# Optimization experiments

Hardware: AMD Instinct MI355X
Metric: run time of the kernel (lower is better)

Reference implementation:

```python
import jax, jax.numpy as jnp
import numpy as np

D_MODEL = 1024
N_HEAD = 16
D_HEAD = D_MODEL // N_HEAD
N_EXPERTS = 8
TOP_K = 2
D_FF = 4096
EPS = 1e-6


def setup_inputs() -> dict:
    key = jax.random.key(0)
    ks = jax.random.split(key, 16)
    s = 0.02  # init scale
    d, dff, E = D_MODEL, D_FF, N_EXPERTS
    return {
        "dec": jax.random.normal(ks[0], (4, 1024, d), jnp.float32),
        "text_encoder": jax.random.normal(ks[1], (4, 512, d), jnp.float32),
        # self-attention projections
        "Wq1": jax.random.normal(ks[2], (d, d), jnp.float32) * s,
        "Wk1": jax.random.normal(ks[3], (d, d), jnp.float32) * s,
        "Wv1": jax.random.normal(ks[4], (d, d), jnp.float32) * s,
        "Wo1": jax.random.normal(ks[5], (d, d), jnp.float32) * s,
        # cross-attention projections
        "Wq2": jax.random.normal(ks[6], (d, d), jnp.float32) * s,
        "Wk2": jax.random.normal(ks[7], (d, d), jnp.float32) * s,
        "Wv2": jax.random.normal(ks[8], (d, d), jnp.float32) * s,
        "Wo2": jax.random.normal(ks[9], (d, d), jnp.float32) * s,
        # shared RMSNorm gain (module uses one norm instance three times)
        "g": jnp.ones((d,), jnp.float32),
        # MoE router + per-expert FFN weights
        "Wg": jax.random.normal(ks[10], (d, E), jnp.float32) * s,
        "W1": jax.random.normal(ks[11], (E, d, dff), jnp.float32) * s,
        "W2": jax.random.normal(ks[12], (E, dff, d), jnp.float32) * s,
    }


def rmsnorm(x, g):
    return x * jax.lax.rsqrt(jnp.mean(x * x, axis=-1, keepdims=True) + EPS) * g


def mha(q_in, k_in, v_in, Wq, Wk, Wv, Wo):
    B, Sq, _ = q_in.shape
    Sk = k_in.shape[1]
    q = (q_in @ Wq).reshape(B, Sq, N_HEAD, D_HEAD)
    k = (k_in @ Wk).reshape(B, Sk, N_HEAD, D_HEAD)
    v = (v_in @ Wv).reshape(B, Sk, N_HEAD, D_HEAD)
    scores = jnp.einsum("bqhd,bkhd->bhqk", q, k) / jnp.sqrt(jnp.asarray(D_HEAD, q.dtype))
    attn = jax.nn.softmax(scores, axis=-1)
    out = jnp.einsum("bhqk,bkhd->bqhd", attn, v).reshape(B, Sq, D_MODEL)
    return out @ Wo


def moe(x, Wg, W1, W2):
    # top-k softmax router, renormalized weights; dense per-expert FFN with combine
    probs = jax.nn.softmax(x @ Wg, axis=-1)              # [B,S,E]
    weights, indices = jax.lax.top_k(probs, TOP_K)        # [B,S,k]
    weights = weights / jnp.sum(weights, axis=-1, keepdims=True)
    # combine[t,e] = sum_k weights[t,k] * (indices[t,k]==e)
    combine = jnp.sum(
        jax.nn.one_hot(indices, N_EXPERTS, dtype=x.dtype) * weights[..., None], axis=-2
    )  # [B,S,E]
    out = jnp.zeros_like(x)
    for e in range(N_EXPERTS):  # fixed small expert loop
        h = jax.nn.relu(x @ W1[e]) @ W2[e]
        out = out + combine[..., e:e + 1] * h
    return weights, indices, out


def reference(dec, text_encoder, Wq1, Wk1, Wv1, Wo1, Wq2, Wk2, Wv2, Wo2, g, Wg, W1, W2):
    # self-attention + residual + RMSNorm (dropout p=0 -> identity)
    x = rmsnorm(mha(dec, dec, dec, Wq1, Wk1, Wv1, Wo1) + dec, g)
    # cross-attention + residual + RMSNorm
    x = rmsnorm(mha(x, text_encoder, text_encoder, Wq2, Wk2, Wv2, Wo2) + x, g)
    # MoE FFN + residual + RMSNorm
    weights, indices, y = moe(x, Wg, W1, W2)
    x = rmsnorm(y + x, g)
    return weights, indices, x
```

## Files before the change

### kernel.cpp

```cpp
#include <hip/hip_runtime.h>
#include <stdint.h>

#define D_    1024
#define BB    4
#define SDEC  1024
#define STXT  512
#define TDEC  4096
#define TTXT  2048
#define NH    16
#define DHD   64
#define NE    8
#define DFF   4096
#define NSLOT 8192
#define ND1   8192
#define ND2   4096
#define MOEGRID 512

using u16 = unsigned short;
typedef __attribute__((ext_vector_type(8))) short bf16x8;
typedef __attribute__((ext_vector_type(4))) float f32x4;

__device__ __forceinline__ float bf2f(u16 h) {
    union { unsigned int u; float f; } x; x.u = ((unsigned int)h) << 16; return x.f;
}
__device__ __forceinline__ u16 f2bf(float f) {
    union { float f; unsigned int u; } x; x.f = f;
    unsigned int lsb = (x.u >> 16) & 1u;
    return (u16)((x.u + 0x7fffu + lsb) >> 16);
}

__device__ __forceinline__ void gld16(const u16* g, u16* l) {
    __builtin_amdgcn_global_load_lds((const __attribute__((address_space(1))) void*)g,
                                     (__attribute__((address_space(3))) void*)l,
                                     16, 0, 0);
}

constexpr int BM = 128, BK = 32;

template<int SPLIT, int EPI, int BROWS>
__global__ __launch_bounds__(256) void gemm_bt(
    const u16* __restrict__ AH, const u16* __restrict__ AL,
    const u16* __restrict__ BH, const u16* __restrict__ BL,
    float* __restrict__ Cf, u16* __restrict__ CH, u16* __restrict__ CL,
    int M, int N, int K, int lda, int ldb, int ldc, int nb2,
    long strA1, long strA2, long strB1, long strB2, long strC1, long strC2)
{
    constexpr int WM = (BROWS == 64) ? 2 : 4;
    constexpr int ASZ = BM * BK, BSZ = BROWS * BK;
    __shared__ u16 smem[(SPLIT ? 2 : 1) * (ASZ + BSZ)];
    u16* sAH = smem;
    u16* sBH = smem + ASZ;
    u16* sAL = SPLIT ? smem + ASZ + BSZ : nullptr;
    u16* sBL = SPLIT ? smem + 2 * ASZ + BSZ : nullptr;

    const int z = blockIdx.z;
    const int z1 = z / nb2, z2 = z % nb2;
    const long zA = (long)z1 * strA1 + (long)z2 * strA2;
    const long zB = (long)z1 * strB1 + (long)z2 * strB2;
    const long zC = (long)z1 * strC1 + (long)z2 * strC2;

    const int tileM = blockIdx.y * BM, tileN = blockIdx.x * BROWS;
    const int t = threadIdx.x;
    const int sr = t >> 2;
    const int sc = (t & 3) << 3;
    const u16* pA = AH + zA + (long)(tileM + sr) * lda + sc;
    const u16* pB = BH + zB + (long)(tileN + sr) * ldb + sc;
    const u16* pAl = nullptr; const u16* pBl = nullptr;
    if constexpr (SPLIT) {
        pAl = AL + zA + (long)(tileM + sr) * lda + sc;
        pBl = BL + zB + (long)(tileN + sr) * ldb + sc;
    }
    const long hA = 64L * lda, hB = 64L * ldb;

    const int lane = t & 63;
    const int wv = t >> 6;
    const int wr = (BROWS == 64) ? (wv << 5) : ((wv >> 1) << 6);
    const int wc = (BROWS == 64) ? 0 : ((wv & 1) << 6);
    const int fr = lane & 15, kg = lane >> 4;

    f32x4 acc[WM][4];
    const f32x4 vzero = {0.f, 0.f, 0.f, 0.f};
#pragma unroll
    for (int m = 0; m < WM; ++m)
#pragma unroll
        for (int n = 0; n < 4; ++n) acc[m][n] = vzero;

    for (int k0 = 0; k0 < K; k0 += BK) {
        gld16(pA + k0,      sAH + t * 8);
        gld16(pA + k0 + hA, sAH + 2048 + t * 8);
        gld16(pB + k0,      sBH + t * 8);
        if constexpr (BROWS == 128) gld16(pB + k0 + hB, sBH + 2048 + t * 8);
        if constexpr (SPLIT) {
            gld16(pAl + k0,      sAL + t * 8);
            gld16(pAl + k0 + hA, sAL + 2048 + t * 8);
            gld16(pBl + k0,      sBL + t * 8);
            if constexpr (BROWS == 128) gld16(pBl + k0 + hB, sBL + 2048 + t * 8);
        }
        __syncthreads();

        bf16x8 fa[WM], fb[4], fal[WM], fbl[4];
#pragma unroll
        for (int m = 0; m < WM; ++m) {
            fa[m] = *(const bf16x8*)&sAH[(wr + m * 16 + fr) * BK + (kg << 3)];
            if constexpr (SPLIT) fal[m] = *(const bf16x8*)&sAL[(wr + m * 16 + fr) * BK + (kg << 3)];
        }
#pragma unroll
        for (int n = 0; n < 4; ++n) {
            fb[n] = *(const bf16x8*)&sBH[(wc + n * 16 + fr) * BK + (kg << 3)];
            if constexpr (SPLIT) fbl[n] = *(const bf16x8*)&sBL[(wc + n * 16 + fr) * BK + (kg << 3)];
        }
#pragma unroll
        for (int m = 0; m < WM; ++m)
#pragma unroll
            for (int n = 0; n < 4; ++n) {
                acc[m][n] = __builtin_amdgcn_mfma_f32_16x16x32_bf16(fa[m], fb[n], acc[m][n], 0, 0, 0);
                if constexpr (SPLIT) {
                    acc[m][n] = __builtin_amdgcn_mfma_f32_16x16x32_bf16(fa[m],  fbl[n], acc[m][n], 0, 0, 0);
                    acc[m][n] = __builtin_amdgcn_mfma_f32_16x16x32_bf16(fal[m], fb[n],  acc[m][n], 0, 0, 0);
                }
            }
        __syncthreads();
    }

#pragma unroll
    for (int m = 0; m < WM; ++m) {
        const int r0 = tileM + wr + m * 16 + (kg << 2);
#pragma unroll
        for (int n = 0; n < 4; ++n) {
            const int col = tileN + wc + n * 16 + fr;
            if (col >= N) continue;
#pragma unroll
            for (int i = 0; i < 4; ++i) {
                const int r = r0 + i;
                if (r >= M) continue;
                const float v = acc[m][n][i];
                const long off = zC + (long)r * ldc + col;
                if constexpr (EPI == 0) {
                    Cf[off] = v;
                } else if constexpr (EPI == 1) {
                    const u16 h = f2bf(v);
                    CH[off] = h;
                    CL[off] = f2bf(v - bf2f(h));
                } else {
                    CH[off] = f2bf(fmaxf(v, 0.f));
                }
            }
        }
    }
}

__global__ __launch_bounds__(256) void pv_gemm(
    const u16* __restrict__ PHp, const u16* __restrict__ PLp,
    const u16* __restrict__ VTH, const u16* __restrict__ VTL,
    float* __restrict__ Op, int Skv, int NZ)
{
    __shared__ u16 smem[12288];
    u16* sAH = smem;
    u16* sAL = smem + 4096;
    u16* sBH = smem + 8192;
    u16* sBL = smem + 10240;

    const int kq = blockIdx.x;
    const int tileM = blockIdx.y * 128;
    const int z = blockIdx.z;
    const int kbase = kq * (Skv >> 2);
    const int nks = Skv >> 7;

    const int t = threadIdx.x;
    const int sr = t >> 2, sc = (t & 3) << 3;
    const u16* pA  = PHp + (long)z * 1024 * Skv + (long)(tileM + sr) * Skv + kbase + sc;
    const u16* pAl = PLp + (long)z * 1024 * Skv + (long)(tileM + sr) * Skv + kbase + sc;
    const u16* pB  = VTH + (long)z * 64 * Skv + (long)sr * Skv + kbase + sc;
    const u16* pBl = VTL + (long)z * 64 * Skv + (long)sr * Skv + kbase + sc;
    const long hA = 64L * Skv;

    const int lane = t & 63, wv = t >> 6;
    const int wr = wv << 5;
    const int fr = lane & 15, kg = lane >> 4;

    f32x4 acc[2][4];
    const f32x4 vzero = {0.f, 0.f, 0.f, 0.f};
#pragma unroll
    for (int m = 0; m < 2; ++m)
#pragma unroll
        for (int n = 0; n < 4; ++n) acc[m][n] = vzero;

    for (int ks = 0; ks < nks; ++ks) {
        const long k0 = (long)ks << 5;
        gld16(pA + k0,       sAH + t * 8);
        gld16(pA + k0 + hA,  sAH + 2048 + t * 8);
        gld16(pAl + k0,      sAL + t * 8);
        gld16(pAl + k0 + hA, sAL + 2048 + t * 8);
        gld16(pB + k0,       sBH + t * 8);
        gld16(pBl + k0,      sBL + t * 8);
        __syncthreads();
        bf16x8 fa[2], fb[4], fal[2], fbl[4];
#pragma unroll
        for (int m = 0; m < 2; ++m) {
            fa[m]  = *(const bf16x8*)&sAH[(wr + m * 16 + fr) * 32 + (kg << 3)];
            fal[m] = *(const bf16x8*)&sAL[(wr + m * 16 + fr) * 32 + (kg << 3)];
        }
#pragma unroll
        for (int n = 0; n < 4; ++n) {
            fb[n]  = *(const bf16x8*)&sBH[(n * 16 + fr) * 32 + (kg << 3)];
            fbl[n] = *(const bf16x8*)&sBL[(n * 16 + fr) * 32 + (kg << 3)];
        }
#pragma unroll
        for (int m = 0; m < 2; ++m)
#pragma unroll
            for (int n = 0; n < 4; ++n) {
                acc[m][n] = __builtin_amdgcn_mfma_f32_16x16x32_bf16(fa[m],  fb[n],  acc[m][n], 0, 0, 0);
                acc[m][n] = __builtin_amdgcn_mfma_f32_16x16x32_bf16(fa[m],  fbl[n], acc[m][n], 0, 0, 0);
                acc[m][n] = __builtin_amdgcn_mfma_f32_16x16x32_bf16(fal[m], fb[n],  acc[m][n], 0, 0, 0);
            }
        __syncthreads();
    }

    const long base = ((long)kq * NZ + z) * 65536;
#pragma unroll
    for (int m = 0; m < 2; ++m) {
        const int r0 = tileM + wr + m * 16 + (kg << 2);
#pragma unroll
        for (int n = 0; n < 4; ++n) {
            const int col = n * 16 + fr;
#pragma unroll
            for (int i = 0; i < 4; ++i)
                Op[base + (long)(r0 + i) * 64 + col] = acc[m][n][i];
        }
    }
}

__global__ __launch_bounds__(256) void pv_combine(
    const float* __restrict__ Op, u16* __restrict__ aoH, u16* __restrict__ aoL,
    int nz, int nh)
{
    const long i = ((long)blockIdx.x * 256 + threadIdx.x) * 4;
    const int zz = (int)(i >> 16);
    const int rem = (int)(i & 65535);
    const int r = rem >> 6, c = rem & 63;
    const int b = zz / nh, h = zz % nh;
    const long kqS = (long)nz * 65536;
    float4 v = *(const float4*)(Op + i);
    const float4 v1 = *(const float4*)(Op + kqS + i);
    const float4 v2 = *(const float4*)(Op + 2 * kqS + i);
    const float4 v3 = *(const float4*)(Op + 3 * kqS + i);
    v.x += v1.x + v2.x + v3.x;
    v.y += v1.y + v2.y + v3.y;
    v.z += v1.z + v2.z + v3.z;
    v.w += v1.w + v2.w + v3.w;
    const long dst = (long)b * SDEC * D_ + (long)r * D_ + h * 64 + c;
    u16 h0 = f2bf(v.x), h1 = f2bf(v.y), h2 = f2bf(v.z), h3 = f2bf(v.w);
    uint2 hh;
    hh.x = (unsigned)h0 | ((unsigned)h1 << 16);
    hh.y = (unsigned)h2 | ((unsigned)h3 << 16);
    *(uint2*)(aoH + dst) = hh;
    u16 l0 = f2bf(v.x - bf2f(h0)), l1 = f2bf(v.y - bf2f(h1));
    u16 l2 = f2bf(v.z - bf2f(h2)), l3 = f2bf(v.w - bf2f(h3));
    uint2 ll;
    ll.x = (unsigned)l0 | ((unsigned)l1 << 16);
    ll.y = (unsigned)l2 | ((unsigned)l3 << 16);
    *(uint2*)(aoL + dst) = ll;
}

template<int EPI>
__global__ __launch_bounds__(256, 2) void moe_gemm2(
    const u16* __restrict__ Ag, int lda,
    const u16* __restrict__ BTbase, int ldb, long btStride,
    float* __restrict__ Cf0, float* __restrict__ Cf1, u16* __restrict__ CH, int ldc,
    const int4* __restrict__ desc, int ndesc, int Kiter)
{
    __shared__ u16 smem[32768];
    const int t = threadIdx.x;
    const int lane = t & 63, wv = t >> 6;
    const int wr = (wv >> 1) << 6, wc = (wv & 1) << 6;
    const int fr = lane & 15, kg = lane >> 4;
    const int nks = Kiter >> 5;

    const int rS = t >> 2;
    const int cS = ((t & 3) ^ ((t >> 3) & 3)) << 3;

    int ldsA[4], ldsB[4];
#pragma unroll
    for (int m = 0; m < 4; ++m) {
        const int ra = wr + m * 16 + fr;
        ldsA[m] = ra * 32 + ((kg ^ ((ra >> 1) & 3)) << 3);
        const int rb = wc + m * 16 + fr;
        ldsB[m] = rb * 32 + ((kg ^ ((rb >> 1) & 3)) << 3);
    }

    for (int p = blockIdx.x; p < ndesc; p += MOEGRID) {
        const int4 d = desc[p];
        if (d.x < 0) continue;
        const int rowbase = d.x, colbase = d.y & 0xFFFF, e = d.y >> 16;
        const int kbase = d.z, s1 = d.w;
        const u16* paS = Ag + (long)(rowbase + rS) * lda + kbase + cS;
        const u16* pbS = BTbase + (long)e * btStride + (long)(colbase + rS) * ldb + kbase + cS;
        const long hA = 64L * lda, hB = 64L * ldb;

        f32x4 acc[4][4];
        const f32x4 vzero = {0.f, 0.f, 0.f, 0.f};
#pragma unroll
        for (int m = 0; m < 4; ++m)
#pragma unroll
            for (int n = 0; n < 4; ++n) acc[m][n] = vzero;

#define STG(ks) { const int s_ = (ks) & 3; const long k0_ = (long)(ks) << 5; \
        u16* b_ = smem + s_ * 8192; \
        gld16(paS + k0_,      b_ + t * 8); \
        gld16(paS + k0_ + hA, b_ + 2048 + t * 8); \
        gld16(pbS + k0_,      b_ + 4096 + t * 8); \
        gld16(pbS + k0_ + hB, b_ + 6144 + t * 8); }

        STG(0); STG(1); STG(2);
        asm volatile("s_waitcnt vmcnt(8)" ::: "memory");
        __builtin_amdgcn_s_barrier();
        __builtin_amdgcn_sched_barrier(0);

        for (int ks = 0; ks < nks; ++ks) {
            if (ks + 3 < nks) STG(ks + 3);
            const u16* sA = smem + (ks & 3) * 8192;
            const u16* sB = sA + 4096;
            bf16x8 fa[4], fb[4];
#pragma unroll
            for (int m = 0; m < 4; ++m) fa[m] = *(const bf16x8*)&sA[ldsA[m]];
#pragma unroll
            for (int n = 0; n < 4; ++n) fb[n] = *(const bf16x8*)&sB[ldsB[n]];
            __builtin_amdgcn_s_setprio(1);
#pragma unroll
            for (int m = 0; m < 4; ++m)
#pragma unroll
                for (int n = 0; n < 4; ++n)
                    acc[m][n] = __builtin_amdgcn_mfma_f32_16x16x32_bf16(fa[m], fb[n], acc[m][n], 0, 0, 0);
            __builtin_amdgcn_s_setprio(0);
            if (ks + 3 < nks)      { asm volatile("s_waitcnt vmcnt(8)" ::: "memory"); }
            else if (ks + 2 < nks) { asm volatile("s_waitcnt vmcnt(4)" ::: "memory"); }
            else                   { asm volatile("s_waitcnt vmcnt(0)" ::: "memory"); }
            __builtin_amdgcn_s_barrier();
            __builtin_amdgcn_sched_barrier(0);
        }
#undef STG

        float* __restrict__ C = (EPI == 0) ? ((kbase == 0) ? Cf0 : Cf1) : nullptr;
#pragma unroll
        for (int m = 0; m < 4; ++m) {
            const int r0 = rowbase + wr + m * 16 + (kg << 2);
#pragma unroll
            for (int n = 0; n < 4; ++n) {
                const int col = colbase + wc + n * 16 + fr;
#pragma unroll
                for (int i = 0; i < 4; ++i) {
                    const int r = r0 + i;
                    if (r >= s1) continue;
                    const float v = acc[m][n][i];
                    const long off = (long)r * ldc + col;
                    if constexpr (EPI == 0) C[off] = v;
                    else                    CH[off] = f2bf(fmaxf(v, 0.f));
                }
            }
        }
    }
}

__global__ __launch_bounds__(256) void split2k(const float* __restrict__ in,
                                               u16* __restrict__ oh, u16* __restrict__ ol, long n)
{
    long i = ((long)blockIdx.x * 256 + threadIdx.x) * 4;
    if (i >= n) return;
    float4 v = *(const float4*)(in + i);
    u16 h0 = f2bf(v.x), h1 = f2bf(v.y), h2 = f2bf(v.z), h3 = f2bf(v.w);
    uint2 oo;
    oo.x = (unsigned)h0 | ((unsigned)h1 << 16);
    oo.y = (unsigned)h2 | ((unsigned)h3 << 16);
    *(uint2*)(oh + i) = oo;
    if (ol) {
        u16 l0 = f2bf(v.x - bf2f(h0)), l1 = f2bf(v.y - bf2f(h1));
        u16 l2 = f2bf(v.z - bf2f(h2)), l3 = f2bf(v.w - bf2f(h3));
        uint2 ll;
        ll.x = (unsigned)l0 | ((unsigned)l1 << 16);
        ll.y = (unsigned)l2 | ((unsigned)l3 << 16);
        *(uint2*)(ol + i) = ll;
    }
}

struct Ptr8 { const float* p[8]; };
__global__ __launch_bounds__(256) void transpose_split_w(
    Ptr8 in, u16* __restrict__ oh, u16* __restrict__ ol)
{
    __shared__ float tile[32][33];
    const int z = blockIdx.z;
    const float* ip = in.p[z];
    u16* ohp = oh + (long)z * D_ * D_;
    u16* olp = ol + (long)z * D_ * D_;
    const int c0 = blockIdx.x * 32, r0 = blockIdx.y * 32;
    const int tx = threadIdx.x & 31, ty = threadIdx.x >> 5;
    for (int i = ty; i < 32; i += 8)
        tile[i][tx] = ip[(long)(r0 + i) * D_ + c0 + tx];
    __syncthreads();
    for (int i = ty; i < 32; i += 8) {
        int oc = c0 + i, orr = r0 + tx;
        float v = tile[tx][i];
        u16 h = f2bf(v);
        ohp[(long)oc * D_ + orr] = h;
        olp[(long)oc * D_ + orr] = f2bf(v - bf2f(h));
    }
}

__global__ __launch_bounds__(256) void transpose_split(
    const float* __restrict__ in, u16* __restrict__ oh, u16* __restrict__ ol,
    int R, int C, int ild, long ibs1, long ibs2, int nb2, int old_, long obs)
{
    __shared__ float tile[32][33];
    const int z = blockIdx.z;
    const float* ip = in + (long)(z / nb2) * ibs1 + (long)(z % nb2) * ibs2;
    u16* ohp = oh + (long)z * obs;
    u16* olp = ol ? ol + (long)z * obs : nullptr;
    const int c0 = blockIdx.x * 32, r0 = blockIdx.y * 32;
    const int tx = threadIdx.x & 31, ty = threadIdx.x >> 5;
    for (int i = ty; i < 32; i += 8) {
        int r = r0 + i, c = c0 + tx;
        tile[i][tx] = (r < R && c < C) ? ip[(long)r * ild + c] : 0.f;
    }
    __syncthreads();
    for (int i = ty; i < 32; i += 8) {
        int oc = c0 + i, orr = r0 + tx;
        if (oc < C && orr < R) {
            float v = tile[tx][i];
            u16 h = f2bf(v);
            ohp[(long)oc * old_ + orr] = h;
            if (olp) olp[(long)oc * old_ + orr] = f2bf(v - bf2f(h));
        }
    }
}

__global__ __launch_bounds__(256) void transpose_split_hl(
    const u16* __restrict__ inH, const u16* __restrict__ inL,
    u16* __restrict__ oh, u16* __restrict__ ol,
    int R, int C, int ild, long ibs1, long ibs2, int nb2, int old_, long obs)
{
    __shared__ float tile[32][33];
    const int z = blockIdx.z;
    const long base = (long)(z / nb2) * ibs1 + (long)(z % nb2) * ibs2;
    u16* ohp = oh + (long)z * obs;
    u16* olp = ol + (long)z * obs;
    const int c0 = blockIdx.x * 32, r0 = blockIdx.y * 32;
    const int tx = threadIdx.x & 31, ty = threadIdx.x >> 5;
    for (int i = ty; i < 32; i += 8) {
        int r = r0 + i, c = c0 + tx;
        float v = 0.f;
        if (r < R && c < C) {
            const long o = base + (long)r * ild + c;
            v = bf2f(inH[o]) + bf2f(inL[o]);
        }
        tile[i][tx] = v;
    }
    __syncthreads();
    for (int i = ty; i < 32; i += 8) {
        int oc = c0 + i, orr = r0 + tx;
        if (oc < C && orr < R) {
            float v = tile[tx][i];
            u16 h = f2bf(v);
            ohp[(long)oc * old_ + orr] = h;
            olp[(long)oc * old_ + orr] = f2bf(v - bf2f(h));
        }
    }
}

__global__ __launch_bounds__(256) void softmax_hl(
    u16* __restrict__ ph, u16* __restrict__ pl, int cols, float scale)
{
    u16* php = ph + (long)blockIdx.x * cols;
    u16* plp = pl + (long)blockIdx.x * cols;
    const int t = threadIdx.x;
    float v[4];
    int vpt;
    if (cols == 1024) {
        vpt = 4;
        uint2 hh = ((const uint2*)php)[t];
        uint2 ll = ((const uint2*)plp)[t];
        v[0] = (bf2f((u16)(hh.x & 0xffff)) + bf2f((u16)(ll.x & 0xffff))) * scale;
        v[1] = (bf2f((u16)(hh.x >> 16))    + bf2f((u16)(ll.x >> 16)))    * scale;
        v[2] = (bf2f((u16)(hh.y & 0xffff)) + bf2f((u16)(ll.y & 0xffff))) * scale;
        v[3] = (bf2f((u16)(hh.y >> 16))    + bf2f((u16)(ll.y >> 16)))    * scale;
    } else {
        vpt = 2;
        unsigned hh = ((const unsigned*)php)[t];
        unsigned ll = ((const unsigned*)plp)[t];
        v[0] = (bf2f((u16)(hh & 0xffff)) + bf2f((u16)(ll & 0xffff))) * scale;
        v[1] = (bf2f((u16)(hh >> 16))    + bf2f((u16)(ll >> 16)))    * scale;
        v[2] = -3.4e38f; v[3] = -3.4e38f;
    }
    float mx = fmaxf(fmaxf(v[0], v[1]), fmaxf(v[2], v[3]));
#pragma unroll
    for (int o = 32; o; o >>= 1) mx = fmaxf(mx, __shfl_xor(mx, o));
    __shared__ float sm[4];
    const int wv = t >> 6, ln = t & 63;
    if (ln == 0) sm[wv] = mx;
    __syncthreads();
    mx = fmaxf(fmaxf(sm[0], sm[1]), fmaxf(sm[2], sm[3]));
    float sum = 0.f;
    for (int i = 0; i < vpt; ++i) { v[i] = expf(v[i] - mx); sum += v[i]; }
#pragma unroll
    for (int o = 32; o; o >>= 1) sum += __shfl_xor(sum, o);
    __shared__ float ss[4];
    if (ln == 0) ss[wv] = sum;
    __syncthreads();
    sum = ss[0] + ss[1] + ss[2] + ss[3];
    const float inv = 1.f / sum;
    if (cols == 1024) {
        float q0 = v[0] * inv, q1 = v[1] * inv, q2 = v[2] * inv, q3 = v[3] * inv;
        u16 h0 = f2bf(q0), h1 = f2bf(q1), h2 = f2bf(q2), h3 = f2bf(q3);
        uint2 hh; hh.x = (unsigned)h0 | ((unsigned)h1 << 16); hh.y = (unsigned)h2 | ((unsigned)h3 << 16);
        ((uint2*)php)[t] = hh;
        u16 l0 = f2bf(q0 - bf2f(h0)), l1 = f2bf(q1 - bf2f(h1));
        u16 l2 = f2bf(q2 - bf2f(h2)), l3 = f2bf(q3 - bf2f(h3));
        uint2 llo; llo.x = (unsigned)l0 | ((unsigned)l1 << 16); llo.y = (unsigned)l2 | ((unsigned)l3 << 16);
        ((uint2*)plp)[t] = llo;
    } else {
        float q0 = v[0] * inv, q1 = v[1] * inv;
        u16 h0 = f2bf(q0), h1 = f2bf(q1);
        ((unsigned*)php)[t] = (unsigned)h0 | ((unsigned)h1 << 16);
        u16 l0 = f2bf(q0 - bf2f(h0)), l1 = f2bf(q1 - bf2f(h1));
        ((unsigned*)plp)[t] = (unsigned)l0 | ((unsigned)l1 << 16);
    }
}

__global__ __launch_bounds__(256) void add_rmsnorm(
    const float* __restrict__ a, const float* __restrict__ b, const float* __restrict__ g,
    float* __restrict__ xo, u16* __restrict__ xh, u16* __restrict__ xl)
{
    const long row = blockIdx.x;
    const int t = threadIdx.x;
    const float* pa = a + row * D_;
    const float* pb = b + row * D_;
    float v[4]; double ssq = 0.0;
#pragma unroll
    for (int i = 0; i < 4; ++i) {
        int c = t + (i << 8);
        v[i] = pa[c] + pb[c];
        ssq += (double)v[i] * v[i];
    }
#pragma unroll
    for (int o = 32; o; o >>= 1) ssq += __shfl_xor(ssq, o);
    __shared__ double sd[4];
    if ((t & 63) == 0) sd[t >> 6] = ssq;
    __syncthreads();
    ssq = sd[0] + sd[1] + sd[2] + sd[3];
    const float rs = (float)(1.0 / sqrt(ssq * (1.0 / 1024.0) + 1e-6));
#pragma unroll
    for (int i = 0; i < 4; ++i) {
        int c = t + (i << 8);
        float o = v[i] * rs * g[c];
        xo[row * D_ + c] = o;
        if (xh) {
            u16 h = f2bf(o);
            xh[row * D_ + c] = h;
            if (xl) xl[row * D_ + c] = f2bf(o - bf2f(h));
        }
    }
}

__global__ __launch_bounds__(256) void router_topk(
    const float* __restrict__ x2, const float* __restrict__ Wg,
    float* __restrict__ outw, float* __restrict__ outi,
    int* __restrict__ idx, float* __restrict__ tokw, int* __restrict__ counts, int T)
{
    const int wid = (int)((blockIdx.x * 256 + threadIdx.x) >> 6);
    const int lane = threadIdx.x & 63;
    if (wid >= T) return;
    float acc[NE];
#pragma unroll
    for (int e = 0; e < NE; ++e) acc[e] = 0.f;
    const float* xr = x2 + (long)wid * D_;
    for (int i = 0; i < 16; ++i) {
        float xv = xr[i * 64 + lane];
        const float* wr = Wg + (long)(i * 64 + lane) * NE;
#pragma unroll
        for (int e = 0; e < NE; ++e) acc[e] += xv * wr[e];
    }
#pragma unroll
    for (int e = 0; e < NE; ++e)
#pragma unroll
        for (int o = 32; o; o >>= 1) acc[e] += __shfl_xor(acc[e], o);
    if (lane == 0) {
        float m = acc[0];
#pragma unroll
        for (int e = 1; e < NE; ++e) m = fmaxf(m, acc[e]);
        float p[NE], s = 0.f;
#pragma unroll
        for (int e = 0; e < NE; ++e) { p[e] = expf(acc[e] - m); s += p[e]; }
        const float invs = 1.f / s;
#pragma unroll
        for (int e = 0; e < NE; ++e) p[e] *= invs;
        int e0 = 0;
#pragma unroll
        for (int e = 1; e < NE; ++e) if (p[e] > p[e0]) e0 = e;
        int e1 = (e0 == 0) ? 1 : 0;
#pragma unroll
        for (int e = 0; e < NE; ++e) if (e != e0 && e != e1 && p[e] > p[e1]) e1 = e;
        float w0 = p[e0], w1 = p[e1];
        const float sw = 1.f / (w0 + w1);
        w0 *= sw; w1 *= sw;
        outw[2 * wid] = w0;      outw[2 * wid + 1] = w1;
        outi[2 * wid] = (float)e0; outi[2 * wid + 1] = (float)e1;
        idx[2 * wid] = e0;       idx[2 * wid + 1] = e1;
        tokw[2 * wid] = w0;      tokw[2 * wid + 1] = w1;
        atomicAdd(&counts[e0], 1);
        atomicAdd(&counts[e1], 1);
    }
}

__global__ void scan_desc(const int* __restrict__ counts, int* __restrict__ cursor,
                          int4* __restrict__ d1, int4* __restrict__ d2)
{
    __shared__ int sseg[NE + 1];
    if (threadIdx.x == 0) {
        int a = 0;
        for (int e = 0; e < NE; ++e) { sseg[e] = a; cursor[e] = a; a += counts[e]; }
        sseg[NE] = a;
    }
    __syncthreads();
    const int e = threadIdx.x;
    if (e < NE) {
        const int s0 = sseg[e], s1 = sseg[e + 1];
        const int nyt = (s1 - s0 + 127) >> 7;
        for (int xt = 0; xt < 32; ++xt)
            for (int yt = 0; yt < nyt; ++yt)
                d1[e + 8 * (xt * nyt + yt)] =
                    make_int4(s0 + yt * 128, (xt * 128) | (e << 16), 0, s1);
        for (int kh = 0; kh < 2; ++kh)
            for (int xt = 0; xt < 8; ++xt)
                for (int yt = 0; yt < nyt; ++yt)
                    d2[e + 8 * ((kh * 8 + xt) * nyt + yt)] =
                        make_int4(s0 + yt * 128, (xt * 128) | (e << 16), kh * 2048, s1);
    }
}

__global__ __launch_bounds__(256) void scatter_slots(
    const int* __restrict__ idx, int* __restrict__ cursor,
    int* __restrict__ row_token, int* __restrict__ slot_of, int T)
{
    const int t = blockIdx.x * 256 + threadIdx.x;
    if (t >= T) return;
#pragma unroll
    for (int k = 0; k < 2; ++k) {
        const int e = idx[2 * t + k];
        const int pos = atomicAdd(&cursor[e], 1);
        row_token[pos] = t;
        slot_of[2 * t + k] = pos;
    }
}

__global__ __launch_bounds__(256) void gather_bf16(
    const float* __restrict__ x2, const int* __restrict__ row_token, u16* __restrict__ Xg)
{
    const int r = blockIdx.x;
    const int t = threadIdx.x;
    const float* src = x2 + (long)row_token[r] * D_ + t * 4;
    float4 v = *(const float4*)src;
    uint2 oo;
    oo.x = (unsigned)f2bf(v.x) | ((unsigned)f2bf(v.y) << 16);
    oo.y = (unsigned)f2bf(v.z) | ((unsigned)f2bf(v.w) << 16);
    *(uint2*)(Xg + (long)r * D_ + t * 4) = oo;
}

__global__ __launch_bounds__(256) void combine_rmsnorm(
    const float* __restrict__ Y0, const float* __restrict__ Y1,
    const int* __restrict__ slot_of, const float* __restrict__ tokw,
    const float* __restrict__ x2, const float* __restrict__ g, float* __restrict__ out)
{
    const long tr = blockIdx.x;
    const int t = threadIdx.x;
    const int s0 = slot_of[2 * tr], s1 = slot_of[2 * tr + 1];
    const float w0 = tokw[2 * tr], w1 = tokw[2 * tr + 1];
    const float* ya0 = Y0 + (long)s0 * D_;
    const float* yb0 = Y1 + (long)s0 * D_;
    const float* ya1 = Y0 + (long)s1 * D_;
    const float* yb1 = Y1 + (long)s1 * D_;
    const float* xr = x2 + tr * D_;
    float v[4]; double ssq = 0.0;
#pragma unroll
    for (int i = 0; i < 4; ++i) {
        int c = t + (i << 8);
        v[i] = w0 * (ya0[c] + yb0[c]) + w1 * (ya1[c] + yb1[c]) + xr[c];
        ssq += (double)v[i] * v[i];
    }
#pragma unroll
    for (int o = 32; o; o >>= 1) ssq += __shfl_xor(ssq, o);
    __shared__ double sd[4];
    if ((t & 63) == 0) sd[t >> 6] = ssq;
    __syncthreads();
    ssq = sd[0] + sd[1] + sd[2] + sd[3];
    const float rs = (float)(1.0 / sqrt(ssq * (1.0 / 1024.0) + 1e-6));
#pragma unroll
    for (int i = 0; i < 4; ++i) {
        int c = t + (i << 8);
        out[tr * D_ + c] = v[i] * rs * g[c];
    }
}

__global__ void sentinel(float* o) { o[0] = 12345.0f; }

extern "C" void kernel_launch(void* const* d_in, const int* in_sizes, int n_in,
                              void* d_out, int out_size, void* d_ws, size_t ws_size,
                              hipStream_t stream)
{
    const float* dec = (const float*)d_in[0];
    const float* te  = (const float*)d_in[1];
    const float* g  = (const float*)d_in[10];
    const float* Wg = (const float*)d_in[11];
    const float* W1 = (const float*)d_in[12];
    const float* W2 = (const float*)d_in[13];
    float* outw = (float*)d_out;
    float* outi = outw + 2 * TDEC;
    float* outx = outw + 4 * TDEC;

    char* ws = (char*)d_ws;
    size_t off = 0;
    auto A = [&](size_t bytes) -> char* {
        char* p = ws + off;
        off += (bytes + 255) & ~(size_t)255;
        return p;
    };

    u16* decH = (u16*)A((size_t)TDEC * D_ * 2);
    u16* decL = (u16*)A((size_t)TDEC * D_ * 2);
    u16* teH  = (u16*)A((size_t)TTXT * D_ * 2);
    u16* teL  = (u16*)A((size_t)TTXT * D_ * 2);
    u16* wtHall = (u16*)A((size_t)8 * D_ * D_ * 2);
    u16* wtLall = (u16*)A((size_t)8 * D_ * D_ * 2);
    float* x1f = (float*)A((size_t)TDEC * D_ * 4);
    float* x2f = (float*)A((size_t)TDEC * D_ * 4);
    float* tokw = (float*)A(NSLOT * 4);
    int* idx    = (int*)A(NSLOT * 4);
    int* counts = (int*)A(256);
    int* cursor = (int*)A(256);
    int* row_token = (int*)A(NSLOT * 4);
    int* slot_of   = (int*)A(NSLOT * 4);
    int4* desc1 = (int4*)A((size_t)ND1 * 16);
    int4* desc2 = (int4*)A((size_t)ND2 * 16);
    const size_t Rbase = off;

    u16* W1T  = (u16*)A((size_t)NE * DFF * D_ * 2);
    u16* W2T  = (u16*)A((size_t)NE * D_ * DFF * 2);
    u16* Xg   = (u16*)A((size_t)(NSLOT + 256) * D_ * 2);
    u16* Hb   = (u16*)A((size_t)(NSLOT + 256) * DFF * 2);
    float* Yseg = (float*)A((size_t)NSLOT * D_ * 4);
    float* Ypart1 = (float*)W1T;
    const size_t moeEnd = off;

    auto allocAttn = [&](bool batched, u16*& PH, u16*& PL, u16*& qkvH, u16*& qkvL,
                         u16*& q2H, u16*& q2L, u16*& kv2H, u16*& kv2L,
                         u16*& vTH, u16*& vTL, u16*& aoH, u16*& aoL,
                         u16*& x1H, u16*& x1L, float*& of, float*& Opart) {
        off = Rbase;
        const size_t pcell = batched ? (size_t)BB * NH * SDEC * SDEC * 2
                                     : (size_t)NH * SDEC * SDEC * 2;
        PH = (u16*)A(pcell);
        PL = (u16*)A(pcell);
        qkvH = (u16*)A((size_t)TDEC * 3 * D_ * 2);
        qkvL = (u16*)A((size_t)TDEC * 3 * D_ * 2);
        q2H  = (u16*)A((size_t)TDEC * D_ * 2);
        q2L  = (u16*)A((size_t)TDEC * D_ * 2);
        kv2H = (u16*)A((size_t)TTXT * 2 * D_ * 2);
        kv2L = (u16*)A((size_t)TTXT * 2 * D_ * 2);
        vTH = (u16*)A((size_t)TDEC * D_ * 2);
        vTL = (u16*)A((size_t)TDEC * D_ * 2);
        aoH = (u16*)A((size_t)TDEC * D_ * 2);
        aoL = (u16*)A((size_t)TDEC * D_ * 2);
        x1H = (u16*)A((size_t)TDEC * D_ * 2);
        x1L = (u16*)A((size_t)TDEC * D_ * 2);
        of  = (float*)A((size_t)TDEC * D_ * 4);
        Opart = (float*)A((size_t)4 * (batched ? BB * NH : NH) * SDEC * DHD * 4);
        return off;
    };

    u16 *PH, *PL, *qkvH, *qkvL, *q2H, *q2L, *kv2H, *kv2L, *vTH, *vTL, *aoH, *aoL, *x1H, *x1L;
    float *of, *Opart;
    size_t attnEnd = allocAttn(true, PH, PL, qkvH, qkvL, q2H, q2L, kv2H, kv2L,
                               vTH, vTL, aoH, aoL, x1H, x1L, of, Opart);
    bool batched = ws_size >= (attnEnd > moeEnd ? attnEnd : moeEnd);
    if (!batched) {
        attnEnd = allocAttn(false, PH, PL, qkvH, qkvL, q2H, q2L, kv2H, kv2L,
                            vTH, vTL, aoH, aoL, x1H, x1L, of, Opart);
        if (ws_size < (attnEnd > moeEnd ? attnEnd : moeEnd)) {
            sentinel<<<1, 1, 0, stream>>>(outw);
            return;
        }
    }

    const dim3 blk(256);

    split2k<<<dim3((TDEC * D_) / 1024), blk, 0, stream>>>(dec, decH, decL, (long)TDEC * D_);
    split2k<<<dim3((TTXT * D_) / 1024), blk, 0, stream>>>(te, teH, teL, (long)TTXT * D_);
    Ptr8 wp;
    for (int i = 0; i < 8; ++i) wp.p[i] = (const float*)d_in[2 + i];
    transpose_split_w<<<dim3(32, 32, 8), blk, 0, stream>>>(wp, wtHall, wtLall);

    gemm_bt<1, 1, 64><<<dim3(48, 32, 1), blk, 0, stream>>>(decH, decL, wtHall, wtLall,
        nullptr, qkvH, qkvL, TDEC, 3 * D_, D_, D_, D_, 3 * D_, 1, 0, 0, 0, 0, 0, 0);
    transpose_split_hl<<<dim3(2, 32, BB * NH), blk, 0, stream>>>(qkvH + 2 * D_, qkvL + 2 * D_,
        vTH, vTL, SDEC, DHD, 3 * D_, (long)SDEC * 3 * D_, DHD, NH, SDEC, (long)DHD * SDEC);

    if (batched) {
        gemm_bt<1, 1, 128><<<dim3(8, 8, BB * NH), blk, 0, stream>>>(
            qkvH, qkvL, qkvH + D_, qkvL + D_, nullptr, PH, PL,
            SDEC, SDEC, DHD, 3 * D_, 3 * D_, SDEC, NH,
            (long)SDEC * 3 * D_, DHD, (long)SDEC * 3 * D_, DHD,
            (long)NH * SDEC * SDEC, (long)SDEC * SDEC);
        softmax_hl<<<dim3(BB * NH * SDEC), blk, 0, stream>>>(PH, PL, SDEC, 0.125f);
        pv_gemm<<<dim3(4, 8, BB * NH), blk, 0, stream>>>(PH, PL, vTH, vTL, Opart, SDEC, BB * NH);
        pv_combine<<<dim3(BB * NH * 64), blk, 0, stream>>>(Opart, aoH, aoL, BB * NH, NH);
    } else {
        for (int b = 0; b < BB; ++b) {
            const long qo3 = (long)b * SDEC * 3 * D_;
            const long qo  = (long)b * SDEC * D_;
            gemm_bt<1, 1, 128><<<dim3(8, 8, NH), blk, 0, stream>>>(
                qkvH + qo3, qkvL + qo3, qkvH + qo3 + D_, qkvL + qo3 + D_,
                nullptr, PH, PL, SDEC, SDEC, DHD, 3 * D_, 3 * D_, SDEC, NH,
                0, DHD, 0, DHD, 0, (long)SDEC * SDEC);
            softmax_hl<<<dim3(NH * SDEC), blk, 0, stream>>>(PH, PL, SDEC, 0.125f);
            pv_gemm<<<dim3(4, 8, NH), blk, 0, stream>>>(PH, PL,
                vTH + (long)b * NH * DHD * SDEC, vTL + (long)b * NH * DHD * SDEC,
                Opart, SDEC, NH);
            pv_combine<<<dim3(NH * 64), blk, 0, stream>>>(Opart, aoH + qo, aoL + qo, NH, NH);
        }
    }
    gemm_bt<1, 0, 64><<<dim3(16, 32, 1), blk, 0, stream>>>(aoH, aoL,
        wtHall + (size_t)3 * D_ * D_, wtLall + (size_t)3 * D_ * D_,
        of, nullptr, nullptr, TDEC, D_, D_, D_, D_, D_, 1, 0, 0, 0, 0, 0, 0);
    add_rmsnorm<<<dim3(TDEC), blk, 0, stream>>>(of, dec, g, x1f, x1H, x1L);

    gemm_bt<1, 1, 64><<<dim3(16, 32, 1), blk, 0, stream>>>(x1H, x1L,
        wtHall + (size_t)4 * D_ * D_, wtLall + (size_t)4 * D_ * D_,
        nullptr, q2H, q2L, TDEC, D_, D_, D_, D_, D_, 1, 0, 0, 0, 0, 0, 0);
    gemm_bt<1, 1, 64><<<dim3(32, 16, 1), blk, 0, stream>>>(teH, teL,
        wtHall + (size_t)5 * D_ * D_, wtLall + (size_t)5 * D_ * D_,
        nullptr, kv2H, kv2L, TTXT, 2 * D_, D_, D_, D_, 2 * D_, 1, 0, 0, 0, 0, 0, 0);
    transpose_split_hl<<<dim3(2, 16, BB * NH), blk, 0, stream>>>(kv2H + D_, kv2L + D_,
        vTH, vTL, STXT, DHD, 2 * D_, (long)STXT * 2 * D_, DHD, NH, STXT, (long)DHD * STXT);

    if (batched) {
        gemm_bt<1, 1, 128><<<dim3(4, 8, BB * NH), blk, 0, stream>>>(
            q2H, q2L, kv2H, kv2L, nullptr, PH, PL,
            SDEC, STXT, DHD, D_, 2 * D_, STXT, NH,
            (long)SDEC * D_, DHD, (long)STXT * 2 * D_, DHD,
            (long)NH * SDEC * STXT, (long)SDEC * STXT);
        softmax_hl<<<dim3(BB * NH * SDEC), blk, 0, stream>>>(PH, PL, STXT, 0.125f);
        pv_gemm<<<dim3(4, 8, BB * NH), blk, 0, stream>>>(PH, PL, vTH, vTL, Opart, STXT, BB * NH);
        pv_combine<<<dim3(BB * NH * 64), blk, 0, stream>>>(Opart, aoH, aoL, BB * NH, NH);
    } else {
        for (int b = 0; b < BB; ++b) {
            const long qo  = (long)b * SDEC * D_;
            const long ko2 = (long)b * STXT * 2 * D_;
            gemm_bt<1, 1, 128><<<dim3(4, 8, NH), blk, 0, stream>>>(
                q2H + qo, q2L + qo, kv2H + ko2, kv2L + ko2,
                nullptr, PH, PL, SDEC, STXT, DHD, D_, 2 * D_, STXT, NH,
                0, DHD, 0, DHD, 0, (long)SDEC * STXT);
            softmax_hl<<<dim3(NH * SDEC), blk, 0, stream>>>(PH, PL, STXT, 0.125f);
            pv_gemm<<<dim3(4, 8, NH), blk, 0, stream>>>(PH, PL,
                vTH + (long)b * NH * DHD * STXT, vTL + (long)b * NH * DHD * STXT,
                Opart, STXT, NH);
            pv_combine<<<dim3(NH * 64), blk, 0, stream>>>(Opart, aoH + qo, aoL + qo, NH, NH);
        }
    }
    gemm_bt<1, 0, 64><<<dim3(16, 32, 1), blk, 0, stream>>>(aoH, aoL,
        wtHall + (size_t)7 * D_ * D_, wtLall + (size_t)7 * D_ * D_,
        of, nullptr, nullptr, TDEC, D_, D_, D_, D_, D_, 1, 0, 0, 0, 0, 0, 0);
    add_rmsnorm<<<dim3(TDEC), blk, 0, stream>>>(of, x1f, g, x2f, nullptr, nullptr);

    hipMemsetAsync(counts, 0, 32, stream);
    hipMemsetAsync(desc1, 0xFF, (size_t)ND1 * 16, stream);
    hipMemsetAsync(desc2, 0xFF, (size_t)ND2 * 16, stream);
    router_topk<<<dim3(TDEC / 4), blk, 0, stream>>>(x2f, Wg, outw, outi, idx, tokw, counts, TDEC);
    scan_desc<<<1, 64, 0, stream>>>(counts, cursor, desc1, desc2);
    scatter_slots<<<dim3(TDEC / 256), blk, 0, stream>>>(idx, cursor, row_token, slot_of, TDEC);
    gather_bf16<<<dim3(NSLOT), blk, 0, stream>>>(x2f, row_token, Xg);

    transpose_split<<<dim3(DFF / 32, D_ / 32, NE), blk, 0, stream>>>(W1, W1T, nullptr,
        D_, DFF, DFF, (long)D_ * DFF, 0, 1, D_, (long)DFF * D_);
    transpose_split<<<dim3(D_ / 32, DFF / 32, NE), blk, 0, stream>>>(W2, W2T, nullptr,
        DFF, D_, D_, (long)D_ * DFF, 0, 1, DFF, (long)D_ * DFF);
    moe_gemm2<2><<<dim3(MOEGRID), blk, 0, stream>>>(Xg, D_, W1T, D_, (long)DFF * D_,
        nullptr, nullptr, Hb, DFF, desc1, ND1, 1024);
    moe_gemm2<0><<<dim3(MOEGRID), blk, 0, stream>>>(Hb, DFF, W2T, DFF, (long)D_ * DFF,
        Yseg, Ypart1, nullptr, D_, desc2, ND2, 2048);
    combine_rmsnorm<<<dim3(TDEC), blk, 0, stream>>>(Yseg, Ypart1, slot_of, tokw, x2f, g, outx);

    (void)in_sizes; (void)n_in; (void)out_size;
}
```

Measured before the change: 1.346 ms.

## Add specialized K=64 attention score and PV kernels with swizzled LDS

Replaces the generic gemm_bt for QK^T scores with a dedicated kernel that loads the full K=64 head dimension into shared memory once, using an XOR-swizzled layout, and runs all MFMAs after a single barrier. The PV kernel now stages 64-wide K chunks per round instead of 32, halving the number of barriers and loop iterations, and also uses the swizzled LDS layout to avoid bank conflicts. Shared memory per block grows, which may reduce how many blocks fit on each CU.

```diff
diff --git a/kernel.cpp b/kernel.cpp
--- a/kernel.cpp
+++ b/kernel.cpp
@@ -149,70 +149,180 @@
     }
 }
 
-__global__ __launch_bounds__(256) void pv_gemm(
-    const u16* __restrict__ PHp, const u16* __restrict__ PLp,
-    const u16* __restrict__ VTH, const u16* __restrict__ VTL,
-    float* __restrict__ Op, int Skv, int NZ)
-{
-    __shared__ u16 smem[12288];
+__global__ __launch_bounds__(256) void scores_k64(
+    const u16* __restrict__ AH, const u16* __restrict__ AL,
+    const u16* __restrict__ BH, const u16* __restrict__ BL,
+    u16* __restrict__ CH, u16* __restrict__ CL,
+    int lda, int ldb, int ldc, int nb2,
+    long strA1, long strA2, long strB1, long strB2, long strC1, long strC2)
+{
+    __shared__ u16 smem[4 * 8192];
     u16* sAH = smem;
-    u16* sAL = smem + 4096;
-    u16* sBH = smem + 8192;
-    u16* sBL = smem + 10240;
-
-    const int kq = blockIdx.x;
-    const int tileM = blockIdx.y * 128;
+    u16* sAL = smem + 8192;
+    u16* sBH = smem + 16384;
+    u16* sBL = smem + 24576;
+
     const int z = blockIdx.z;
-    const int kbase = kq * (Skv >> 2);
-    const int nks = Skv >> 7;
-
+    const int z1 = z / nb2, z2 = z % nb2;
+    const long zA = (long)z1 * strA1 + (long)z2 * strA2;
+    const long zB = (long)z1 * strB1 + (long)z2 * strB2;
+    const long zC = (long)z1 * strC1 + (long)z2 * strC2;
+
+    const int tileM = blockIdx.y * 128, tileN = blockIdx.x * 128;
     const int t = threadIdx.x;
-    const int sr = t >> 2, sc = (t & 3) << 3;
-    const u16* pA  = PHp + (long)z * 1024 * Skv + (long)(tileM + sr) * Skv + kbase + sc;
-    const u16* pAl = PLp + (long)z * 1024 * Skv + (long)(tileM + sr) * Skv + kbase + sc;
-    const u16* pB  = VTH + (long)z * 64 * Skv + (long)sr * Skv + kbase + sc;
-    const u16* pBl = VTL + (long)z * 64 * Skv + (long)sr * Skv + kbase + sc;
-    const long hA = 64L * Skv;
-
-    const int lane = t & 63, wv = t >> 6;
-    const int wr = wv << 5;
+    const int srow = t >> 3;
+    const int scol = ((t & 7) ^ (srow & 7)) << 3;
+    const u16* pA  = AH + zA + (long)(tileM + srow) * lda + scol;
+    const u16* pAl = AL + zA + (long)(tileM + srow) * lda + scol;
+    const u16* pB  = BH + zB + (long)(tileN + srow) * ldb + scol;
+    const u16* pBl = BL + zB + (long)(tileN + srow) * ldb + scol;
+
+#pragma unroll
+    for (int c = 0; c < 4; ++c) {
+        const long ro = 32L * c * lda;
+        const long rb = 32L * c * ldb;
+        gld16(pA  + ro, sAH + c * 2048 + t * 8);
+        gld16(pAl + ro, sAL + c * 2048 + t * 8);
+        gld16(pB  + rb, sBH + c * 2048 + t * 8);
+        gld16(pBl + rb, sBL + c * 2048 + t * 8);
+    }
+    __syncthreads();
+
+    const int lane = t & 63;
+    const int wv = t >> 6;
+    const int wr = (wv >> 1) << 6, wc = (wv & 1) << 6;
     const int fr = lane & 15, kg = lane >> 4;
 
-    f32x4 acc[2][4];
+    f32x4 acc[4][4];
     const f32x4 vzero = {0.f, 0.f, 0.f, 0.f};
 #pragma unroll
-    for (int m = 0; m < 2; ++m)
+    for (int m = 0; m < 4; ++m)
 #pragma unroll
         for (int n = 0; n < 4; ++n) acc[m][n] = vzero;
 
-    for (int ks = 0; ks < nks; ++ks) {
-        const long k0 = (long)ks << 5;
-        gld16(pA + k0,       sAH + t * 8);
-        gld16(pA + k0 + hA,  sAH + 2048 + t * 8);
-        gld16(pAl + k0,      sAL + t * 8);
-        gld16(pAl + k0 + hA, sAL + 2048 + t * 8);
-        gld16(pB + k0,       sBH + t * 8);
-        gld16(pBl + k0,      sBL + t * 8);
-        __syncthreads();
-        bf16x8 fa[2], fb[4], fal[2], fbl[4];
-#pragma unroll
-        for (int m = 0; m < 2; ++m) {
-            fa[m]  = *(const bf16x8*)&sAH[(wr + m * 16 + fr) * 32 + (kg << 3)];
-            fal[m] = *(const bf16x8*)&sAL[(wr + m * 16 + fr) * 32 + (kg << 3)];
+#pragma unroll
+    for (int ks = 0; ks < 2; ++ks) {
+        bf16x8 fa[4], fb[4], fal[4], fbl[4];
+#pragma unroll
+        for (int m = 0; m < 4; ++m) {
+            const int r = wr + m * 16 + fr;
+            const int o = r * 64 + (((kg | (ks << 2)) ^ (r & 7)) << 3);
+            fa[m]  = *(const bf16x8*)&sAH[o];
+            fal[m] = *(const bf16x8*)&sAL[o];
         }
 #pragma unroll
         for (int n = 0; n < 4; ++n) {
-            fb[n]  = *(const bf16x8*)&sBH[(n * 16 + fr) * 32 + (kg << 3)];
-            fbl[n] = *(const bf16x8*)&sBL[(n * 16 + fr) * 32 + (kg << 3)];
-        }
-#pragma unroll
-        for (int m = 0; m < 2; ++m)
+            const int r = wc + n * 16 + fr;
+            const int o = r * 64 + (((kg | (ks << 2)) ^ (r & 7)) << 3);
+            fb[n]  = *(const bf16x8*)&sBH[o];
+            fbl[n] = *(const bf16x8*)&sBL[o];
+        }
+#pragma unroll
+        for (int m = 0; m < 4; ++m)
 #pragma unroll
             for (int n = 0; n < 4; ++n) {
                 acc[m][n] = __builtin_amdgcn_mfma_f32_16x16x32_bf16(fa[m],  fb[n],  acc[m][n], 0, 0, 0);
                 acc[m][n] = __builtin_amdgcn_mfma_f32_16x16x32_bf16(fa[m],  fbl[n], acc[m][n], 0, 0, 0);
                 acc[m][n] = __builtin_amdgcn_mfma_f32_16x16x32_bf16(fal[m], fb[n],  acc[m][n], 0, 0, 0);
             }
+    }
+
+#pragma unroll
+    for (int m = 0; m < 4; ++m) {
+        const int r0 = tileM + wr + m * 16 + (kg << 2);
+#pragma unroll
+        for (int n = 0; n < 4; ++n) {
+            const int col = tileN + wc + n * 16 + fr;
+#pragma unroll
+            for (int i = 0; i < 4; ++i) {
+                const float v = acc[m][n][i];
+                const long off = zC + (long)(r0 + i) * ldc + col;
+                const u16 h = f2bf(v);
+                CH[off] = h;
+                CL[off] = f2bf(v - bf2f(h));
+            }
+        }
+    }
+}
+
+__global__ __launch_bounds__(256) void pv_k64(
+    const u16* __restrict__ PHp, const u16* __restrict__ PLp,
+    const u16* __restrict__ VTH, const u16* __restrict__ VTL,
+    float* __restrict__ Op, int Skv, int NZ)
+{
+    __shared__ u16 smem[24576];
+    u16* sAH = smem;
+    u16* sAL = smem + 8192;
+    u16* sBH = smem + 16384;
+    u16* sBL = smem + 20480;
+
+    const int kq = blockIdx.x;
+    const int tileM = blockIdx.y * 128;
+    const int z = blockIdx.z;
+    const int kbase = kq * (Skv >> 2);
+    const int nrounds = Skv >> 8;
+
+    const int t = threadIdx.x;
+    const int srow = t >> 3;
+    const int scol = ((t & 7) ^ (srow & 7)) << 3;
+    const u16* pA  = PHp + (long)z * 1024 * Skv + (long)(tileM + srow) * Skv + kbase + scol;
+    const u16* pAl = PLp + (long)z * 1024 * Skv + (long)(tileM + srow) * Skv + kbase + scol;
+    const u16* pB  = VTH + (long)z * 64 * Skv + (long)srow * Skv + kbase + scol;
+    const u16* pBl = VTL + (long)z * 64 * Skv + (long)srow * Skv + kbase + scol;
+
+    const int lane = t & 63, wv = t >> 6;
+    const int wr = wv << 5;
+    const int fr = lane & 15, kg = lane >> 4;
+
+    f32x4 acc[2][4];
+    const f32x4 vzero = {0.f, 0.f, 0.f, 0.f};
+#pragma unroll
+    for (int m = 0; m < 2; ++m)
+#pragma unroll
+        for (int n = 0; n < 4; ++n) acc[m][n] = vzero;
+
+    for (int rr = 0; rr < nrounds; ++rr) {
+        const long k0 = (long)rr << 6;
+#pragma unroll
+        for (int c = 0; c < 4; ++c) {
+            const long ro = 32L * c * Skv;
+            gld16(pA  + k0 + ro, sAH + c * 2048 + t * 8);
+            gld16(pAl + k0 + ro, sAL + c * 2048 + t * 8);
+        }
+#pragma unroll
+        for (int c = 0; c < 2; ++c) {
+            const long ro = 32L * c * Skv;
+            gld16(pB  + k0 + ro, sBH + c * 2048 + t * 8);
+            gld16(pBl + k0 + ro, sBL + c * 2048 + t * 8);
+        }
+        __syncthreads();
+
+#pragma unroll
+        for (int ks = 0; ks < 2; ++ks) {
+            bf16x8 fa[2], fb[4], fal[2], fbl[4];
+#pragma unroll
+            for (int m = 0; m < 2; ++m) {
+                const int r = wr + m * 16 + fr;
+                const int o = r * 64 + (((kg | (ks << 2)) ^ (r & 7)) << 3);
+                fa[m]  = *(const bf16x8*)&sAH[o];
+                fal[m] = *(const bf16x8*)&sAL[o];
+            }
+#pragma unroll
+            for (int n = 0; n < 4; ++n) {
+                const int r = n * 16 + fr;
+                const int o = r * 64 + (((kg | (ks << 2)) ^ (r & 7)) << 3);
+                fb[n]  = *(const bf16x8*)&sBH[o];
+                fbl[n] = *(const bf16x8*)&sBL[o];
+            }
+#pragma unroll
+            for (int m = 0; m < 2; ++m)
+#pragma unroll
+                for (int n = 0; n < 4; ++n) {
+                    acc[m][n] = __builtin_amdgcn_mfma_f32_16x16x32_bf16(fa[m],  fb[n],  acc[m][n], 0, 0, 0);
+                    acc[m][n] = __builtin_amdgcn_mfma_f32_16x16x32_bf16(fa[m],  fbl[n], acc[m][n], 0, 0, 0);
+                    acc[m][n] = __builtin_amdgcn_mfma_f32_16x16x32_bf16(fal[m], fb[n],  acc[m][n], 0, 0, 0);
+                }
+        }
         __syncthreads();
     }
 
@@ -802,24 +912,24 @@
         vTH, vTL, SDEC, DHD, 3 * D_, (long)SDEC * 3 * D_, DHD, NH, SDEC, (long)DHD * SDEC);
 
     if (batched) {
-        gemm_bt<1, 1, 128><<<dim3(8, 8, BB * NH), blk, 0, stream>>>(
-            qkvH, qkvL, qkvH + D_, qkvL + D_, nullptr, PH, PL,
-            SDEC, SDEC, DHD, 3 * D_, 3 * D_, SDEC, NH,
+        scores_k64<<<dim3(8, 8, BB * NH), blk, 0, stream>>>(
+            qkvH, qkvL, qkvH + D_, qkvL + D_, PH, PL,
+            3 * D_, 3 * D_, SDEC, NH,
             (long)SDEC * 3 * D_, DHD, (long)SDEC * 3 * D_, DHD,
             (long)NH * SDEC * SDEC, (long)SDEC * SDEC);
         softmax_hl<<<dim3(BB * NH * SDEC), blk, 0, stream>>>(PH, PL, SDEC, 0.125f);
-        pv_gemm<<<dim3(4, 8, BB * NH), blk, 0, stream>>>(PH, PL, vTH, vTL, Opart, SDEC, BB * NH);
+        pv_k64<<<dim3(4, 8, BB * NH), blk, 0, stream>>>(PH, PL, vTH, vTL, Opart, SDEC, BB * NH);
         pv_combine<<<dim3(BB * NH * 64), blk, 0, stream>>>(Opart, aoH, aoL, BB * NH, NH);
     } else {
         for (int b = 0; b < BB; ++b) {
             const long qo3 = (long)b * SDEC * 3 * D_;
             const long qo  = (long)b * SDEC * D_;
-            gemm_bt<1, 1, 128><<<dim3(8, 8, NH), blk, 0, stream>>>(
+            scores_k64<<<dim3(8, 8, NH), blk, 0, stream>>>(
                 qkvH + qo3, qkvL + qo3, qkvH + qo3 + D_, qkvL + qo3 + D_,
-                nullptr, PH, PL, SDEC, SDEC, DHD, 3 * D_, 3 * D_, SDEC, NH,
+                PH, PL, 3 * D_, 3 * D_, SDEC, NH,
                 0, DHD, 0, DHD, 0, (long)SDEC * SDEC);
             softmax_hl<<<dim3(NH * SDEC), blk, 0, stream>>>(PH, PL, SDEC, 0.125f);
-            pv_gemm<<<dim3(4, 8, NH), blk, 0, stream>>>(PH, PL,
+            pv_k64<<<dim3(4, 8, NH), blk, 0, stream>>>(PH, PL,
                 vTH + (long)b * NH * DHD * SDEC, vTL + (long)b * NH * DHD * SDEC,
                 Opart, SDEC, NH);
             pv_combine<<<dim3(NH * 64), blk, 0, stream>>>(Opart, aoH + qo, aoL + qo, NH, NH);
@@ -840,24 +950,24 @@
         vTH, vTL, STXT, DHD, 2 * D_, (long)STXT * 2 * D_, DHD, NH, STXT, (long)DHD * STXT);
 
     if (batched) {
-        gemm_bt<1, 1, 128><<<dim3(4, 8, BB * NH), blk, 0, stream>>>(
-            q2H, q2L, kv2H, kv2L, nullptr, PH, PL,
-            SDEC, STXT, DHD, D_, 2 * D_, STXT, NH,
+        scores_k64<<<dim3(4, 8, BB * NH), blk, 0, stream>>>(
+            q2H, q2L, kv2H, kv2L, PH, PL,
+            D_, 2 * D_, STXT, NH,
             (long)SDEC * D_, DHD, (long)STXT * 2 * D_, DHD,
             (long)NH * SDEC * STXT, (long)SDEC * STXT);
         softmax_hl<<<dim3(BB * NH * SDEC), blk, 0, stream>>>(PH, PL, STXT, 0.125f);
-        pv_gemm<<<dim3(4, 8, BB * NH), blk, 0, stream>>>(PH, PL, vTH, vTL, Opart, STXT, BB * NH);
+        pv_k64<<<dim3(4, 8, BB * NH), blk, 0, stream>>>(PH, PL, vTH, vTL, Opart, STXT, BB * NH);
         pv_combine<<<dim3(BB * NH * 64), blk, 0, stream>>>(Opart, aoH, aoL, BB * NH, NH);
     } else {
         for (int b = 0; b < BB; ++b) {
             const long qo  = (long)b * SDEC * D_;
             const long ko2 = (long)b * STXT * 2 * D_;
-            gemm_bt<1, 1, 128><<<dim3(4, 8, NH), blk, 0, stream>>>(
+            scores_k64<<<dim3(4, 8, NH), blk, 0, stream>>>(
                 q2H + qo, q2L + qo, kv2H + ko2, kv2L + ko2,
-                nullptr, PH, PL, SDEC, STXT, DHD, D_, 2 * D_, STXT, NH,
+                PH, PL, D_, 2 * D_, STXT, NH,
                 0, DHD, 0, DHD, 0, (long)SDEC * STXT);
             softmax_hl<<<dim3(NH * SDEC), blk, 0, stream>>>(PH, PL, STXT, 0.125f);
-            pv_gemm<<<dim3(4, 8, NH), blk, 0, stream>>>(PH, PL,
+            pv_k64<<<dim3(4, 8, NH), blk, 0, stream>>>(PH, PL,
                 vTH + (long)b * NH * DHD * STXT, vTL + (long)b * NH * DHD * STXT,
                 Opart, STXT, NH);
             pv_combine<<<dim3(NH * 64), blk, 0, stream>>>(Opart, aoH + qo, aoL + qo, NH, NH);
```

After: 1.299 ms (median of 2 runs). 3.5% less time.
